# Kernel optimization log

Measured on AMD Instinct MI355X. Metric: run time of the kernel, lower is better.

## Reference

```python
import jax, jax.numpy as jnp
import numpy as np

N_NODES = 50000
N_EDGES = 600000
NUM_RELS = 5
IN_CH = 768
HID = 128
OUT_CH = 128
REL_DIM = 200


def _segment_softmax(scores, seg, n):
    # numerically stable softmax over variable-size segments (destination nodes)
    m = jax.ops.segment_max(scores, seg, num_segments=n)
    e = jnp.exp(scores - m[seg])
    s = jax.ops.segment_sum(e, seg, num_segments=n)
    return e / s[seg]


def _hgn_conv(x, edge_index, edge_type, W, Wr, a, Wres, rel_tab, final):
    # x: [N, h_in]; W: [h, h_in]; Wr: [h, rel_dim]; a: [3h]; rel_tab: [R, rel_dim]
    src = edge_index[0]
    dst = edge_index[1]
    n = x.shape[0]
    h = W.shape[0]
    Wx = x @ W.T                      # [N, h] (shared by x_i, x_j, messages)
    rel = rel_tab[edge_type] @ Wr.T   # [E, h]
    aA, aB, aC = a[:h], a[h:2 * h], a[2 * h:]
    # a([Wx_i | Wx_j | Wr rel]) decomposed to avoid materializing the concat
    score = Wx[dst] @ aA + Wx[src] @ aB + rel @ aC   # [E]
    alpha = jax.nn.leaky_relu(score, 0.2)
    alpha = _segment_softmax(alpha, dst, n)
    agg = jax.ops.segment_sum(Wx[src] * alpha[:, None], dst, num_segments=n)
    out = jax.nn.elu(agg + x @ Wres.T)
    if final:
        out = out / jnp.maximum(jnp.linalg.norm(out, axis=1, keepdims=True), 1e-12)
    return out, alpha


def setup_inputs() -> dict:
    key = jax.random.key(0)
    ks = jax.random.split(key, 20)
    s = 0.02
    return {
        "x": jax.random.normal(ks[0], (N_NODES, IN_CH), jnp.float32),
        "edge_index": jax.random.randint(ks[1], (2, N_EDGES), 0, N_NODES, jnp.int64 if jax.config.jax_enable_x64 else jnp.int32),
        "edge_type": jax.random.randint(ks[2], (N_EDGES,), 0, NUM_RELS, jnp.int64 if jax.config.jax_enable_x64 else jnp.int32),
        "l1_W": jax.random.normal(ks[3], (HID, IN_CH), jnp.float32) * s,
        "l1_b": jnp.zeros((HID,), jnp.float32),
        "l2_W": jax.random.normal(ks[4], (OUT_CH, HID), jnp.float32) * s,
        "l2_b": jnp.zeros((OUT_CH,), jnp.float32),
        "W1": jax.random.normal(ks[5], (HID, HID), jnp.float32) * s,
        "Wr1": jax.random.normal(ks[6], (HID, REL_DIM), jnp.float32) * s,
        "a1": jax.random.normal(ks[7], (3 * HID,), jnp.float32) * s,
        "Wres1": jax.random.normal(ks[8], (HID, HID), jnp.float32) * s,
        "rel1": jax.random.normal(ks[9], (NUM_RELS, REL_DIM), jnp.float32),
        "W2": jax.random.normal(ks[10], (HID, HID), jnp.float32) * s,
        "Wr2": jax.random.normal(ks[11], (HID, REL_DIM), jnp.float32) * s,
        "a2": jax.random.normal(ks[12], (3 * HID,), jnp.float32) * s,
        "Wres2": jax.random.normal(ks[13], (HID, HID), jnp.float32) * s,
        "rel2": jax.random.normal(ks[14], (NUM_RELS, REL_DIM), jnp.float32),
    }


def reference(x, edge_index, edge_type, l1_W, l1_b, l2_W, l2_b,
              W1, Wr1, a1, Wres1, rel1, W2, Wr2, a2, Wres2, rel2):
    out = jax.nn.leaky_relu(x @ l1_W.T + l1_b, 0.01)
    # layer 1 (dropout is identity in eval mode)
    out, alpha = _hgn_conv(out, edge_index, edge_type, W1, Wr1, a1, Wres1, rel1, final=False)
    # layer 2: original code blends alpha into self.alpha but weights messages
    # with its own (unblended) softmax alpha, so pre_alpha does not affect output
    out, _ = _hgn_conv(out, edge_index, edge_type, W2, Wr2, a2, Wres2, rel2, final=True)
    out = jax.nn.leaky_relu(out @ l2_W.T + l2_b, 0.01)
    return out
```

## Files before the change

### kernel.cpp

```cpp
#include <hip/hip_runtime.h>

namespace {

typedef unsigned short ushort_t;
typedef unsigned int uint_t;
typedef __attribute__((ext_vector_type(8))) short bf16x8;
typedef __attribute__((ext_vector_type(4))) float f32x4;

constexpr int N   = 50000;
constexpr int E   = 600000;
constexpr int NR  = 5;
constexpr int KIN = 768;
constexpr int H   = 128;
constexpr int RD  = 200;

__device__ inline ushort_t f2b(float f){
  uint_t u = __builtin_bit_cast(uint_t, f);
  uint_t r = (u + 0x7FFFu + ((u >> 16) & 1u)) >> 16;
  return (ushort_t)r;
}
__device__ inline float b2f_lo(uint_t u){ return __builtin_bit_cast(float, u << 16); }
__device__ inline float b2f_hi(uint_t u){ return __builtin_bit_cast(float, u & 0xFFFF0000u); }
__device__ inline float b2f_us(ushort_t h){ return __builtin_bit_cast(float, ((uint_t)h) << 16); }
__device__ inline uint_t cvtpk(float lo, float hi){
  uint_t r;
  asm("v_cvt_pk_bf16_f32 %0, %1, %2" : "=v"(r) : "v"(lo), "v"(hi));
  return r;
}

__global__ void prep_k(const float* __restrict__ l1W, const float* __restrict__ W1,
                       const float* __restrict__ R1, const float* __restrict__ W2,
                       const float* __restrict__ R2, const float* __restrict__ l2W,
                       ushort_t* __restrict__ wts, int* __restrict__ deg,
                       const int* __restrict__ edst,
                       const float* __restrict__ rel1, const float* __restrict__ Wr1,
                       const float* __restrict__ a1, float* __restrict__ sC1,
                       const float* __restrict__ rel2, const float* __restrict__ Wr2,
                       const float* __restrict__ a2, float* __restrict__ sC2){
  constexpr int S0 = H * KIN;
  constexpr int S1 = H * H;
  int b = blockIdx.x, tid = threadIdx.x;
  if (b < 704){
    int i = b * 256 + tid;
    float v;
    if (i < S0) v = l1W[i];
    else {
      int j = i - S0, seg = j >> 14, off = j & (S1 - 1);
      const float* srcs[5] = {W1, R1, W2, R2, l2W};
      v = srcs[seg][off];
    }
    wts[i] = f2b(v);
  } else if (b < 706){
    int L = b - 704;
    const float* rel = L ? rel2 : rel1;
    const float* Wr  = L ? Wr2  : Wr1;
    const float* a   = L ? a2   : a1;
    float*       sC  = L ? sC2  : sC1;
    __shared__ float red[256];
    int n = tid >> 1, half = tid & 1;
    float aC = a[256 + n];
    for (int r = 0; r < NR; ++r){
      float p = 0.f;
      for (int k = half * 100; k < half * 100 + 100; ++k)
        p += rel[r * RD + k] * Wr[n * RD + k];
      red[tid] = p * aC;
      __syncthreads();
      for (int s = 128; s > 0; s >>= 1){
        if (tid < s) red[tid] += red[tid + s];
        __syncthreads();
      }
      if (tid == 0) sC[r] = red[0];
      __syncthreads();
    }
  } else {
    int e = (b - 706) * 256 + tid;
    if (e < E) atomicAdd(&deg[edst[e]], 1);
  }
}

__global__ void scan1_k(const int* __restrict__ deg, int* __restrict__ chunk,
                        int* __restrict__ bsums, int n){
  __shared__ int s[256];
  int tid = threadIdx.x, i = blockIdx.x * 256 + tid;
  int v = (i < n) ? deg[i] : 0;
  s[tid] = v; __syncthreads();
  for (int off = 1; off < 256; off <<= 1){
    int t = (tid >= off) ? s[tid - off] : 0;
    __syncthreads();
    s[tid] += t;
    __syncthreads();
  }
  if (i < n) chunk[i] = s[tid] - v;
  if (tid == 255) bsums[blockIdx.x] = s[255];
}

__global__ void scan2_k(const int* __restrict__ bsums, int* __restrict__ boffs, int nb){
  __shared__ int s[256];
  int tid = threadIdx.x;
  int v = (tid < nb) ? bsums[tid] : 0;
  s[tid] = v; __syncthreads();
  for (int off = 1; off < 256; off <<= 1){
    int t = (tid >= off) ? s[tid - off] : 0;
    __syncthreads();
    s[tid] += t;
    __syncthreads();
  }
  if (tid < nb) boffs[tid] = s[tid] - v;
}

__global__ void scan3_k(int* __restrict__ rowptr, const int* __restrict__ boffs,
                        int* __restrict__ cursor, int n, int total){
  int i = blockIdx.x * 256 + threadIdx.x;
  if (i < n){
    int v = rowptr[i] + boffs[blockIdx.x];
    rowptr[i] = v; cursor[i] = v;
  }
  if (i == 0) rowptr[n] = total;
}

__global__ void fill_k(const int* __restrict__ src, const int* __restrict__ dst,
                       const int* __restrict__ et, int* __restrict__ cursor,
                       int* __restrict__ cpk){
  int e = blockIdx.x * 256 + threadIdx.x;
  if (e < E){
    int d = dst[e];
    int p = atomicAdd(&cursor[d], 1);
    cpk[p] = src[e] | (et[e] << 16);
  }
}

template<int K1, int M1, bool AFP32, bool NORM, bool STORE1, int M2>
__device__ __forceinline__ void gfused_impl(
    const void* __restrict__ Ap, const ushort_t* __restrict__ Wb1,
    const float* __restrict__ bias1,
    const ushort_t* __restrict__ WxG, const int* __restrict__ rowptr,
    const int* __restrict__ cpk, const float* __restrict__ sAi,
    const float* __restrict__ sBi, const float* __restrict__ sCi,
    ushort_t* __restrict__ out1,
    const ushort_t* __restrict__ Wb2, const float* __restrict__ vec2,
    void* __restrict__ out2, float* __restrict__ sAo, float* __restrict__ sBo, int M)
{
  constexpr int BK = 64;
  constexpr int NT = K1 / BK;
  constexpr int SP = 72;
  constexpr int CP = 136;
  __shared__ __align__(16) ushort_t U[128 * CP];
  __shared__ __align__(16) ushort_t Cs[64 * CP];
  ushort_t* const As  = U;
  ushort_t* const Bs  = U + 64 * SP;
  ushort_t* const B2s = U;
  const int tid  = threadIdx.x;
  const int wave = tid >> 6, lane = tid & 63;
  const int l15  = lane & 15, quad = lane >> 4;
  const int row0 = blockIdx.x * 64;

  if (M1 == 2){
    const int grp = tid >> 4;
    const int l   = tid & 15;
    const int gb  = tid & 48;
    #pragma unroll 1
    for (int nb = 0; nb < 4; ++nb){
      int lrow = nb * 16 + grp;
      int node = row0 + lrow;
      uint4 o = make_uint4(0, 0, 0, 0);
      if (node < M){
        int p0 = rowptr[node], p1 = rowptr[node + 1];
        int dg = p1 - p0;
        float sa = sAi[node];
        float m = -1e30f, ssum = 0.f;
        float a[8];
        #pragma unroll
        for (int j = 0; j < 8; ++j) a[j] = 0.f;
        for (int c0 = 0; c0 < dg; c0 += 16){
          int cnt = dg - c0; if (cnt > 16) cnt = 16;
          bool ok = l < cnt;
          int pk = cpk[p0 + c0 + (ok ? l : 0)];
          float s = sa + sBi[pk & 0xFFFF] + sCi[pk >> 16];
          s = s > 0.f ? s : 0.2f * s;
          float sv = ok ? s : -1e30f;
          #pragma unroll
          for (int off = 8; off > 0; off >>= 1) sv = fmaxf(sv, __shfl_xor(sv, off, 16));
          float mn = fmaxf(m, sv);
          float corr = __expf(m - mn);
          ssum *= corr;
          #pragma unroll
          for (int j = 0; j < 8; ++j) a[j] *= corr;
          float ev = ok ? __expf(s - mn) : 0.f;
          float es = ev;
          #pragma unroll
          for (int off = 8; off > 0; off >>= 1) es += __shfl_xor(es, off, 16);
          ssum += es;
          m = mn;
          int png = ok ? pk : 0;
          for (int e = 0; e < cnt; e += 4){
            int b0l = gb + e;
            int pe0 = __shfl(png, b0l,     64), pe1 = __shfl(png, b0l + 1, 64);
            int pe2 = __shfl(png, b0l + 2, 64), pe3 = __shfl(png, b0l + 3, 64);
            float e0 = __shfl(ev, b0l,     64), e1 = __shfl(ev, b0l + 1, 64);
            float e2 = __shfl(ev, b0l + 2, 64), e3 = __shfl(ev, b0l + 3, 64);
            uint4 u0 = *reinterpret_cast<const uint4*>(WxG + (size_t)(pe0 & 0xFFFF) * 128 + l * 8);
            uint4 u1 = *reinterpret_cast<const uint4*>(WxG + (size_t)(pe1 & 0xFFFF) * 128 + l * 8);
            uint4 u2 = *reinterpret_cast<const uint4*>(WxG + (size_t)(pe2 & 0xFFFF) * 128 + l * 8);
            uint4 u3 = *reinterpret_cast<const uint4*>(WxG + (size_t)(pe3 & 0xFFFF) * 128 + l * 8);
            a[0] += e0 * b2f_lo(u0.x); a[1] += e0 * b2f_hi(u0.x);
            a[2] += e0 * b2f_lo(u0.y); a[3] += e0 * b2f_hi(u0.y);
            a[4] += e0 * b2f_lo(u0.z); a[5] += e0 * b2f_hi(u0.z);
            a[6] += e0 * b2f_lo(u0.w); a[7] += e0 * b2f_hi(u0.w);
            a[0] += e1 * b2f_lo(u1.x); a[1] += e1 * b2f_hi(u1.x);
            a[2] += e1 * b2f_lo(u1.y); a[3] += e1 * b2f_hi(u1.y);
            a[4] += e1 * b2f_lo(u1.z); a[5] += e1 * b2f_hi(u1.z);
            a[6] += e1 * b2f_lo(u1.w); a[7] += e1 * b2f_hi(u1.w);
            a[0] += e2 * b2f_lo(u2.x); a[1] += e2 * b2f_hi(u2.x);
            a[2] += e2 * b2f_lo(u2.y); a[3] += e2 * b2f_hi(u2.y);
            a[4] += e2 * b2f_lo(u2.z); a[5] += e2 * b2f_hi(u2.z);
            a[6] += e2 * b2f_lo(u2.w); a[7] += e2 * b2f_hi(u2.w);
            a[0] += e3 * b2f_lo(u3.x); a[1] += e3 * b2f_hi(u3.x);
            a[2] += e3 * b2f_lo(u3.y); a[3] += e3 * b2f_hi(u3.y);
            a[4] += e3 * b2f_lo(u3.z); a[5] += e3 * b2f_hi(u3.z);
            a[6] += e3 * b2f_lo(u3.w); a[7] += e3 * b2f_hi(u3.w);
          }
        }
        float inv = (dg > 0) ? 1.f / ssum : 0.f;
        o.x = cvtpk(a[0] * inv, a[1] * inv);
        o.y = cvtpk(a[2] * inv, a[3] * inv);
        o.z = cvtpk(a[4] * inv, a[5] * inv);
        o.w = cvtpk(a[6] * inv, a[7] * inv);
      }
      *reinterpret_cast<uint4*>(&Cs[lrow * CP + l * 8]) = o;
    }
  }

  f32x4 acc[8];
  #pragma unroll
  for (int t = 0; t < 8; ++t) acc[t] = (f32x4){0.f, 0.f, 0.f, 0.f};

  const int ar = tid >> 2, aq = tid & 3;
  const int agrow = row0 + ar;
  const bool aok = agrow < M;
  const int awoff = ar * SP + aq * 16;
  const int bn = tid >> 1, bs = (tid & 1) * 32;
  const ushort_t* bsrc = Wb1 + (size_t)bn * K1 + bs;

  float4 pf0, pf1, pf2, pf3;
  uint4  pu0, pu1;
  uint4  pb0, pb1, pb2, pb3;
  pf0 = pf1 = pf2 = pf3 = make_float4(0.f, 0.f, 0.f, 0.f);
  pu0 = pu1 = make_uint4(0, 0, 0, 0);

#define ISSUE_A(kk) do{ if (aok){                                               \
    if constexpr (AFP32){                                                       \
      const float* ap_ = (const float*)Ap + (size_t)agrow * K1 + (kk) + aq * 16; \
      pf0 = *reinterpret_cast<const float4*>(ap_);                              \
      pf1 = *reinterpret_cast<const float4*>(ap_ + 4);                          \
      pf2 = *reinterpret_cast<const float4*>(ap_ + 8);                          \
      pf3 = *reinterpret_cast<const float4*>(ap_ + 12);                         \
    } else {                                                                    \
      const ushort_t* apb_ = (const ushort_t*)Ap + (size_t)agrow * K1 + (kk) + aq * 16; \
      pu0 = *reinterpret_cast<const uint4*>(apb_);                              \
      pu1 = *reinterpret_cast<const uint4*>(apb_ + 8);                          \
    } } }while(0)

#define ISSUE_B(kk) do{                                                         \
    pb0 = *reinterpret_cast<const uint4*>(bsrc + (kk));                         \
    pb1 = *reinterpret_cast<const uint4*>(bsrc + (kk) + 8);                     \
    pb2 = *reinterpret_cast<const uint4*>(bsrc + (kk) + 16);                    \
    pb3 = *reinterpret_cast<const uint4*>(bsrc + (kk) + 24);                    \
  }while(0)

#define WRITE_AB() do{                                                          \
    uint4 av0_, av1_;                                                           \
    if constexpr (AFP32){                                                       \
      av0_.x = cvtpk(pf0.x, pf0.y); av0_.y = cvtpk(pf0.z, pf0.w);               \
      av0_.z = cvtpk(pf1.x, pf1.y); av0_.w = cvtpk(pf1.z, pf1.w);               \
      av1_.x = cvtpk(pf2.x, pf2.y); av1_.y = cvtpk(pf2.z, pf2.w);               \
      av1_.z = cvtpk(pf3.x, pf3.y); av1_.w = cvtpk(pf3.z, pf3.w);               \
    } else { av0_ = pu0; av1_ = pu1; }                                          \
    *reinterpret_cast<uint4*>(&As[awoff])     = av0_;                           \
    *reinterpret_cast<uint4*>(&As[awoff + 8]) = av1_;                           \
    *reinterpret_cast<uint4*>(&Bs[bn * SP + bs])      = pb0;                    \
    *reinterpret_cast<uint4*>(&Bs[bn * SP + bs + 8])  = pb1;                    \
    *reinterpret_cast<uint4*>(&Bs[bn * SP + bs + 16]) = pb2;                    \
    *reinterpret_cast<uint4*>(&Bs[bn * SP + bs + 24]) = pb3;                    \
  }while(0)

  ISSUE_A(0); ISSUE_B(0);
  for (int t = 0; t < NT; ++t){
    WRITE_AB();
    __syncthreads();
    if (t + 1 < NT){ ISSUE_A((t + 1) * BK); ISSUE_B((t + 1) * BK); }
    bf16x8 af0 = *reinterpret_cast<const bf16x8*>(&As[(wave * 16 + l15) * SP + quad * 8]);
    bf16x8 af1 = *reinterpret_cast<const bf16x8*>(&As[(wave * 16 + l15) * SP + 32 + quad * 8]);
    #pragma unroll
    for (int tt = 0; tt < 8; ++tt){
      bf16x8 b0 = *reinterpret_cast<const bf16x8*>(&Bs[(tt * 16 + l15) * SP + quad * 8]);
      acc[tt] = __builtin_amdgcn_mfma_f32_16x16x32_bf16(af0, b0, acc[tt], 0, 0, 0);
      bf16x8 b1 = *reinterpret_cast<const bf16x8*>(&Bs[(tt * 16 + l15) * SP + 32 + quad * 8]);
      acc[tt] = __builtin_amdgcn_mfma_f32_16x16x32_bf16(af1, b1, acc[tt], 0, 0, 0);
    }
    __syncthreads();
  }
#undef ISSUE_A
#undef ISSUE_B
#undef WRITE_AB

  uint4 wreg[8];
  #pragma unroll
  for (int i = 0; i < 8; ++i){
    int idx = tid + 256 * i;
    int rr = idx >> 4, c8 = idx & 15;
    wreg[i] = *reinterpret_cast<const uint4*>(Wb2 + (size_t)rr * 128 + c8 * 8);
  }

  float vv[8][4];
  #pragma unroll
  for (int t = 0; t < 8; ++t){
    #pragma unroll
    for (int r = 0; r < 4; ++r){
      int lr  = wave * 16 + quad * 4 + r;
      int col = t * 16 + l15;
      float v = acc[t][r];
      if (M1 == 1){
        v += bias1[col];
        v = v > 0.f ? v : 0.01f * v;
      } else {
        v += b2f_us(Cs[lr * CP + col]);
        v = v > 0.f ? v : __expf(v) - 1.f;
      }
      vv[t][r] = v;
    }
  }
  #pragma unroll
  for (int i = 0; i < 8; ++i){
    int idx = tid + 256 * i;
    int rr = idx >> 4, c8 = idx & 15;
    *reinterpret_cast<uint4*>(&B2s[rr * CP + c8 * 8]) = wreg[i];
  }
  if (NORM){
    #pragma unroll
    for (int r = 0; r < 4; ++r){
      float ss = 0.f;
      #pragma unroll
      for (int t = 0; t < 8; ++t) ss += vv[t][r] * vv[t][r];
      #pragma unroll
      for (int off = 1; off < 16; off <<= 1) ss += __shfl_xor(ss, off, 64);
      float sc = 1.f / fmaxf(sqrtf(ss), 1e-12f);
      #pragma unroll
      for (int t = 0; t < 8; ++t) vv[t][r] *= sc;
    }
  }
  #pragma unroll
  for (int t = 0; t < 8; t += 2){
    #pragma unroll
    for (int r = 0; r < 4; ++r){
      int lr  = wave * 16 + quad * 4 + r;
      int c0  = t * 16 + l15, c1 = c0 + 16;
      uint_t pr = cvtpk(vv[t][r], vv[t + 1][r]);
      Cs[lr * CP + c0] = (ushort_t)pr;
      Cs[lr * CP + c1] = (ushort_t)(pr >> 16);
      if (STORE1){
        int grow = row0 + lr;
        if (grow < M){
          out1[(size_t)grow * 128 + c0] = (ushort_t)pr;
          out1[(size_t)grow * 128 + c1] = (ushort_t)(pr >> 16);
        }
      }
    }
  }
  __syncthreads();

  #pragma unroll
  for (int t = 0; t < 8; ++t) acc[t] = (f32x4){0.f, 0.f, 0.f, 0.f};
  #pragma unroll
  for (int kk = 0; kk < 4; ++kk){
    bf16x8 af2 = *reinterpret_cast<const bf16x8*>(&Cs[(wave * 16 + l15) * CP + kk * 32 + quad * 8]);
    #pragma unroll
    for (int t = 0; t < 8; ++t){
      bf16x8 bfr = *reinterpret_cast<const bf16x8*>(&B2s[(t * 16 + l15) * CP + kk * 32 + quad * 8]);
      acc[t] = __builtin_amdgcn_mfma_f32_16x16x32_bf16(af2, bfr, acc[t], 0, 0, 0);
    }
  }

  if (M2 == 1){
    #pragma unroll
    for (int t = 0; t < 8; ++t){
      #pragma unroll
      for (int r = 0; r < 4; ++r){
        int grow = row0 + wave * 16 + quad * 4 + r;
        if (grow >= M) continue;
        int col = t * 16 + l15;
        float v = acc[t][r] + vec2[col];
        v = v > 0.f ? v : 0.01f * v;
        ((float*)out2)[(size_t)grow * 128 + col] = v;
      }
    }
  } else {
    #pragma unroll
    for (int t = 0; t < 8; t += 2){
      #pragma unroll
      for (int r = 0; r < 4; ++r){
        int grow = row0 + wave * 16 + quad * 4 + r;
        if (grow >= M) continue;
        int c0 = t * 16 + l15;
        uint_t pr = cvtpk(acc[t][r], acc[t + 1][r]);
        ((ushort_t*)out2)[(size_t)grow * 128 + c0]      = (ushort_t)pr;
        ((ushort_t*)out2)[(size_t)grow * 128 + c0 + 16] = (ushort_t)(pr >> 16);
      }
    }
    #pragma unroll
    for (int r = 0; r < 4; ++r){
      float pa = 0.f, pb = 0.f;
      #pragma unroll
      for (int t = 0; t < 8; ++t){
        int col = t * 16 + l15;
        pa += acc[t][r] * vec2[col];
        pb += acc[t][r] * vec2[128 + col];
      }
      #pragma unroll
      for (int off = 1; off < 16; off <<= 1){
        pa += __shfl_xor(pa, off, 64);
        pb += __shfl_xor(pb, off, 64);
      }
      int grow = row0 + wave * 16 + quad * 4 + r;
      if (l15 == r && grow < M){ sAo[grow] = pa; sBo[grow] = pb; }
    }
  }
}

__global__ __launch_bounds__(256) void g1_k(
    const void* Ap, const ushort_t* Wb1, const float* bias1,
    ushort_t* out1, const ushort_t* Wb2, const float* vec2,
    void* out2, float* sAo, float* sBo, int M){
  gfused_impl<KIN, 1, true, false, true, 3>(Ap, Wb1, bias1, nullptr, nullptr,
      nullptr, nullptr, nullptr, nullptr, out1, Wb2, vec2, out2, sAo, sBo, M);
}
__global__ __launch_bounds__(256) void g2_k(
    const void* Ap, const ushort_t* Wb1,
    const ushort_t* WxG, const int* rowptr, const int* cpk,
    const float* sAi, const float* sBi, const float* sCi,
    ushort_t* out1, const ushort_t* Wb2, const float* vec2,
    void* out2, float* sAo, float* sBo, int M){
  gfused_impl<H, 2, false, false, true, 3>(Ap, Wb1, nullptr, WxG, rowptr, cpk,
      sAi, sBi, sCi, out1, Wb2, vec2, out2, sAo, sBo, M);
}
__global__ __launch_bounds__(256) void g3_k(
    const void* Ap, const ushort_t* Wb1,
    const ushort_t* WxG, const int* rowptr, const int* cpk,
    const float* sAi, const float* sBi, const float* sCi,
    const ushort_t* Wb2, const float* vec2, void* out2, int M){
  gfused_impl<H, 2, false, true, false, 1>(Ap, Wb1, nullptr, WxG, rowptr, cpk,
      sAi, sBi, sCi, nullptr, Wb2, vec2, out2, nullptr, nullptr, M);
}

}

extern "C" void kernel_launch(void* const* d_in, const int* in_sizes, int n_in,
                              void* d_out, int out_size, void* d_ws, size_t ws_size,
                              hipStream_t stream)
{
  const float* x     = (const float*)d_in[0];
  const int*   eidx  = (const int*)d_in[1];
  const int*   et    = (const int*)d_in[2];
  const float* l1W   = (const float*)d_in[3];
  const float* l1b   = (const float*)d_in[4];
  const float* l2W   = (const float*)d_in[5];
  const float* l2b   = (const float*)d_in[6];
  const float* W1    = (const float*)d_in[7];
  const float* Wr1   = (const float*)d_in[8];
  const float* a1    = (const float*)d_in[9];
  const float* Wres1 = (const float*)d_in[10];
  const float* rel1  = (const float*)d_in[11];
  const float* W2    = (const float*)d_in[12];
  const float* Wr2   = (const float*)d_in[13];
  const float* a2    = (const float*)d_in[14];
  const float* Wres2 = (const float*)d_in[15];
  const float* rel2  = (const float*)d_in[16];
  float* outp = (float*)d_out;

  const int* esrc = eidx;
  const int* edst = eidx + E;

  float* f = (float*)d_ws;
  size_t o = 0;
  float* sA1  = f + o; o += N;
  float* sB1  = f + o; o += N;
  float* sA2  = f + o; o += N;
  float* sB2  = f + o; o += N;
  float* sC1  = f + o; o += 8;
  float* sC2  = f + o; o += 8;
  ushort_t* us = (ushort_t*)(f + o);
  size_t ou = 0;
  ushort_t* b0   = us + ou; ou += (size_t)N * H;
  ushort_t* b1   = us + ou; ou += (size_t)N * H;
  ushort_t* WxA  = us + ou; ou += (size_t)N * H;
  ushort_t* WxB  = us + ou; ou += (size_t)N * H;
  ushort_t* wtsb = us + ou; ou += (size_t)H * KIN + 5 * H * H;
  ushort_t* l1Wb = wtsb;
  ushort_t* W1b  = wtsb + H * KIN;
  ushort_t* R1b  = W1b + H * H;
  ushort_t* W2b  = R1b + H * H;
  ushort_t* R2b  = W2b + H * H;
  ushort_t* l2Wb = R2b + H * H;
  if (ou & 1) ou += 1;
  int* wi = (int*)(us + ou);
  size_t oi = 0;
  int* deg    = wi + oi; oi += N;
  int* rowptr = wi + oi; oi += N + 1;
  int* cursor = wi + oi; oi += N;
  int* bsums  = wi + oi; oi += 256;
  int* boffs  = wi + oi; oi += 256;
  int* cpk    = wi + oi; oi += E;

  const int EB    = (E + 255) / 256;
  const int NB256 = (N + 255) / 256;
  const int GB    = (N + 63) / 64;

  hipMemsetAsync(deg, 0, (size_t)N * sizeof(int), stream);
  prep_k<<<706 + EB, 256, 0, stream>>>(l1W, W1, Wres1, W2, Wres2, l2W, wtsb, deg,
                                       edst, rel1, Wr1, a1, sC1, rel2, Wr2, a2, sC2);
  scan1_k<<<NB256, 256, 0, stream>>>(deg, rowptr, bsums, N);
  scan2_k<<<1, 256, 0, stream>>>(bsums, boffs, NB256);
  scan3_k<<<NB256, 256, 0, stream>>>(rowptr, boffs, cursor, N, E);
  fill_k<<<EB, 256, 0, stream>>>(esrc, edst, et, cursor, cpk);

  g1_k<<<GB, 256, 0, stream>>>(x, l1Wb, l1b, b0, W1b, a1, WxA, sA1, sB1, N);

  g2_k<<<GB, 256, 0, stream>>>(b0, R1b, WxA, rowptr, cpk, sA1, sB1, sC1,
                               b1, W2b, a2, WxB, sA2, sB2, N);

  g3_k<<<GB, 256, 0, stream>>>(b1, R2b, WxB, rowptr, cpk, sA2, sB2, sC2,
                               l2Wb, l2b, outp, N);
}
```

Measured before the change: 481.7 us.

## Specialize GEMM kernels, merge scan stages, and restructure residual GEMM ordering

Merges scan2 and scan3 so every block redundantly scans the block sums, removing one kernel launch. Splits the templated fused GEMM into a dedicated layer-1 kernel with a K tile of 128 and wider prefetch, and a layer-2/3 kernel. The layer-2/3 kernel loads the A fragments directly from global memory into registers and runs the residual GEMM before the edge aggregation, so the tiled K loop and its staging go away. Output stores are coalesced through shared memory as 16-byte vectors. In exchange it uses more registers and LDS, and every scan block repeats the same small scan.

```diff
diff --git a/kernel.cpp b/kernel.cpp
--- a/kernel.cpp
+++ b/kernel.cpp
@@ -94,7 +94,8 @@
   if (tid == 255) bsums[blockIdx.x] = s[255];
 }
 
-__global__ void scan2_k(const int* __restrict__ bsums, int* __restrict__ boffs, int nb){
+__global__ void scan3_k(int* __restrict__ rowptr, const int* __restrict__ bsums,
+                        int* __restrict__ cursor, int n, int total, int nb){
   __shared__ int s[256];
   int tid = threadIdx.x;
   int v = (tid < nb) ? bsums[tid] : 0;
@@ -105,15 +106,12 @@
     s[tid] += t;
     __syncthreads();
   }
-  if (tid < nb) boffs[tid] = s[tid] - v;
-}
-
-__global__ void scan3_k(int* __restrict__ rowptr, const int* __restrict__ boffs,
-                        int* __restrict__ cursor, int n, int total){
-  int i = blockIdx.x * 256 + threadIdx.x;
+  int bown = (blockIdx.x < nb) ? bsums[blockIdx.x] : 0;
+  int add  = s[blockIdx.x] - bown;
+  int i = blockIdx.x * 256 + tid;
   if (i < n){
-    int v = rowptr[i] + boffs[blockIdx.x];
-    rowptr[i] = v; cursor[i] = v;
+    int val = rowptr[i] + add;
+    rowptr[i] = val; cursor[i] = val;
   }
   if (i == 0) rowptr[n] = total;
 }
@@ -129,10 +127,167 @@
   }
 }
 
-template<int K1, int M1, bool AFP32, bool NORM, bool STORE1, int M2>
-__device__ __forceinline__ void gfused_impl(
-    const void* __restrict__ Ap, const ushort_t* __restrict__ Wb1,
-    const float* __restrict__ bias1,
+__global__ __launch_bounds__(256) void g1_k(
+    const float* __restrict__ Ap, const ushort_t* __restrict__ Wb1,
+    const float* __restrict__ bias1, ushort_t* __restrict__ out1,
+    const ushort_t* __restrict__ Wb2, const float* __restrict__ vec2,
+    ushort_t* __restrict__ out2, float* __restrict__ sAo, float* __restrict__ sBo, int M)
+{
+  constexpr int K1 = KIN;
+  constexpr int BK = 128;
+  constexpr int NT = K1 / BK;
+  constexpr int SP = 136;
+  __shared__ __align__(16) ushort_t U[192 * SP];
+  __shared__ __align__(16) ushort_t Cs[64 * SP];
+  ushort_t* const As  = U;
+  ushort_t* const Bs  = U + 64 * SP;
+  ushort_t* const B2s = U;
+  const int tid  = threadIdx.x;
+  const int wave = tid >> 6, lane = tid & 63;
+  const int l15  = lane & 15, quad = lane >> 4;
+  const int row0 = blockIdx.x * 64;
+
+  f32x4 acc[8];
+  #pragma unroll
+  for (int t = 0; t < 8; ++t) acc[t] = (f32x4){0.f, 0.f, 0.f, 0.f};
+
+  const int ar = tid >> 2, aseg = (tid & 3) * 32;
+  int agrow = row0 + ar; if (agrow >= M) agrow = M - 1;
+  const float* asrc = Ap + (size_t)agrow * K1 + aseg;
+  const int bn = tid >> 1, bh = (tid & 1) * 64;
+  const ushort_t* bsrc = Wb1 + (size_t)bn * K1 + bh;
+
+  float4 pa[8]; uint4 pb[8];
+#define ISSUE(kk) do{                                                           \
+    _Pragma("unroll") for (int j_ = 0; j_ < 8; ++j_)                            \
+      pa[j_] = *reinterpret_cast<const float4*>(asrc + (kk) + j_ * 4);          \
+    _Pragma("unroll") for (int j_ = 0; j_ < 8; ++j_)                            \
+      pb[j_] = *reinterpret_cast<const uint4*>(bsrc + (kk) + j_ * 8);           \
+  }while(0)
+#define WRITE_AB() do{                                                          \
+    _Pragma("unroll") for (int j_ = 0; j_ < 4; ++j_){                           \
+      uint4 av_;                                                                \
+      av_.x = cvtpk(pa[2*j_].x, pa[2*j_].y);  av_.y = cvtpk(pa[2*j_].z, pa[2*j_].w); \
+      av_.z = cvtpk(pa[2*j_+1].x, pa[2*j_+1].y); av_.w = cvtpk(pa[2*j_+1].z, pa[2*j_+1].w); \
+      *reinterpret_cast<uint4*>(&As[ar * SP + aseg + j_ * 8]) = av_;            \
+    }                                                                           \
+    _Pragma("unroll") for (int j_ = 0; j_ < 8; ++j_)                            \
+      *reinterpret_cast<uint4*>(&Bs[bn * SP + bh + j_ * 8]) = pb[j_];           \
+  }while(0)
+
+  ISSUE(0);
+  for (int t = 0; t < NT; ++t){
+    WRITE_AB();
+    __syncthreads();
+    if (t + 1 < NT) ISSUE((t + 1) * BK);
+    #pragma unroll
+    for (int kk = 0; kk < 4; ++kk){
+      bf16x8 af = *reinterpret_cast<const bf16x8*>(&As[(wave * 16 + l15) * SP + kk * 32 + quad * 8]);
+      #pragma unroll
+      for (int tt = 0; tt < 8; ++tt){
+        bf16x8 bfr = *reinterpret_cast<const bf16x8*>(&Bs[(tt * 16 + l15) * SP + kk * 32 + quad * 8]);
+        acc[tt] = __builtin_amdgcn_mfma_f32_16x16x32_bf16(af, bfr, acc[tt], 0, 0, 0);
+      }
+    }
+    __syncthreads();
+  }
+#undef ISSUE
+#undef WRITE_AB
+
+  uint4 wreg[8];
+  #pragma unroll
+  for (int i = 0; i < 8; ++i){
+    int idx = tid + 256 * i;
+    int rr = idx >> 4, c8 = idx & 15;
+    wreg[i] = *reinterpret_cast<const uint4*>(Wb2 + (size_t)rr * 128 + c8 * 8);
+  }
+
+  const int lr0 = wave * 16 + quad * 4;
+  float vv[8][4];
+  #pragma unroll
+  for (int t = 0; t < 8; ++t){
+    #pragma unroll
+    for (int r = 0; r < 4; ++r){
+      int col = t * 16 + l15;
+      float v = acc[t][r] + bias1[col];
+      vv[t][r] = v > 0.f ? v : 0.01f * v;
+    }
+  }
+  #pragma unroll
+  for (int i = 0; i < 8; ++i){
+    int idx = tid + 256 * i;
+    int rr = idx >> 4, c8 = idx & 15;
+    *reinterpret_cast<uint4*>(&B2s[rr * SP + c8 * 8]) = wreg[i];
+  }
+  #pragma unroll
+  for (int t = 0; t < 8; t += 2){
+    #pragma unroll
+    for (int r = 0; r < 4; ++r){
+      int row = lr0 + r;
+      int c0 = t * 16 + l15, c1 = c0 + 16;
+      uint_t pr = cvtpk(vv[t][r], vv[t + 1][r]);
+      Cs[row * SP + c0] = (ushort_t)pr;
+      Cs[row * SP + c1] = (ushort_t)(pr >> 16);
+    }
+  }
+  __syncthreads();
+
+  #pragma unroll
+  for (int i = 0; i < 4; ++i){
+    int idx = tid + 256 * i;
+    int row = idx >> 4, c8 = idx & 15;
+    int g = row0 + row;
+    if (g < M)
+      *reinterpret_cast<uint4*>(out1 + (size_t)g * 128 + c8 * 8) =
+          *reinterpret_cast<const uint4*>(&Cs[row * SP + c8 * 8]);
+  }
+
+  #pragma unroll
+  for (int t = 0; t < 8; ++t) acc[t] = (f32x4){0.f, 0.f, 0.f, 0.f};
+  #pragma unroll
+  for (int kk = 0; kk < 4; ++kk){
+    bf16x8 af2 = *reinterpret_cast<const bf16x8*>(&Cs[(wave * 16 + l15) * SP + kk * 32 + quad * 8]);
+    #pragma unroll
+    for (int t = 0; t < 8; ++t){
+      bf16x8 bfr = *reinterpret_cast<const bf16x8*>(&B2s[(t * 16 + l15) * SP + kk * 32 + quad * 8]);
+      acc[t] = __builtin_amdgcn_mfma_f32_16x16x32_bf16(af2, bfr, acc[t], 0, 0, 0);
+    }
+  }
+
+  #pragma unroll
+  for (int t = 0; t < 8; t += 2){
+    #pragma unroll
+    for (int r = 0; r < 4; ++r){
+      int grow = row0 + lr0 + r;
+      if (grow >= M) continue;
+      int c0 = t * 16 + l15;
+      uint_t pr = cvtpk(acc[t][r], acc[t + 1][r]);
+      out2[(size_t)grow * 128 + c0]      = (ushort_t)pr;
+      out2[(size_t)grow * 128 + c0 + 16] = (ushort_t)(pr >> 16);
+    }
+  }
+  #pragma unroll
+  for (int r = 0; r < 4; ++r){
+    float pa2 = 0.f, pb2 = 0.f;
+    #pragma unroll
+    for (int t = 0; t < 8; ++t){
+      int col = t * 16 + l15;
+      pa2 += acc[t][r] * vec2[col];
+      pb2 += acc[t][r] * vec2[128 + col];
+    }
+    #pragma unroll
+    for (int off = 1; off < 16; off <<= 1){
+      pa2 += __shfl_xor(pa2, off, 64);
+      pb2 += __shfl_xor(pb2, off, 64);
+    }
+    int grow = row0 + lr0 + r;
+    if (l15 == r && grow < M){ sAo[grow] = pa2; sBo[grow] = pb2; }
+  }
+}
+
+template<bool NORM, bool STORE1, int M2>
+__device__ __forceinline__ void g23_impl(
+    const ushort_t* __restrict__ Ap, const ushort_t* __restrict__ Wb1,
     const ushort_t* __restrict__ WxG, const int* __restrict__ rowptr,
     const int* __restrict__ cpk, const float* __restrict__ sAi,
     const float* __restrict__ sBi, const float* __restrict__ sCi,
@@ -140,24 +295,45 @@
     const ushort_t* __restrict__ Wb2, const float* __restrict__ vec2,
     void* __restrict__ out2, float* __restrict__ sAo, float* __restrict__ sBo, int M)
 {
-  constexpr int BK = 64;
-  constexpr int NT = K1 / BK;
-  constexpr int SP = 72;
-  constexpr int CP = 136;
-  __shared__ __align__(16) ushort_t U[128 * CP];
-  __shared__ __align__(16) ushort_t Cs[64 * CP];
-  ushort_t* const As  = U;
-  ushort_t* const Bs  = U + 64 * SP;
-  ushort_t* const B2s = U;
+  constexpr int SP = 136;
+  __shared__ __align__(16) ushort_t U[128 * SP];
+  __shared__ __align__(16) ushort_t Cs[64 * SP];
   const int tid  = threadIdx.x;
   const int wave = tid >> 6, lane = tid & 63;
   const int l15  = lane & 15, quad = lane >> 4;
   const int row0 = blockIdx.x * 64;
 
-  if (M1 == 2){
-    const int grp = tid >> 4;
-    const int l   = tid & 15;
-    const int gb  = tid & 48;
+  int arl = row0 + wave * 16 + l15; if (arl >= M) arl = M - 1;
+  const ushort_t* arow = Ap + (size_t)arl * 128 + quad * 8;
+  bf16x8 af0 = *reinterpret_cast<const bf16x8*>(arow);
+  bf16x8 af1 = *reinterpret_cast<const bf16x8*>(arow + 32);
+  bf16x8 af2 = *reinterpret_cast<const bf16x8*>(arow + 64);
+  bf16x8 af3 = *reinterpret_cast<const bf16x8*>(arow + 96);
+
+  {
+    const int bn = tid >> 1, bh = (tid & 1) * 64;
+    const ushort_t* bsrc = Wb1 + (size_t)bn * 128 + bh;
+    #pragma unroll
+    for (int j = 0; j < 8; ++j)
+      *reinterpret_cast<uint4*>(&U[bn * SP + bh + j * 8]) =
+          *reinterpret_cast<const uint4*>(bsrc + j * 8);
+  }
+  __syncthreads();
+
+  f32x4 acc[8];
+  #pragma unroll
+  for (int t = 0; t < 8; ++t) acc[t] = (f32x4){0.f, 0.f, 0.f, 0.f};
+  #pragma unroll
+  for (int t = 0; t < 8; ++t){
+    const ushort_t* bp = &U[(t * 16 + l15) * SP + quad * 8];
+    acc[t] = __builtin_amdgcn_mfma_f32_16x16x32_bf16(af0, *reinterpret_cast<const bf16x8*>(bp),      acc[t], 0, 0, 0);
+    acc[t] = __builtin_amdgcn_mfma_f32_16x16x32_bf16(af1, *reinterpret_cast<const bf16x8*>(bp + 32), acc[t], 0, 0, 0);
+    acc[t] = __builtin_amdgcn_mfma_f32_16x16x32_bf16(af2, *reinterpret_cast<const bf16x8*>(bp + 64), acc[t], 0, 0, 0);
+    acc[t] = __builtin_amdgcn_mfma_f32_16x16x32_bf16(af3, *reinterpret_cast<const bf16x8*>(bp + 96), acc[t], 0, 0, 0);
+  }
+
+  {
+    const int grp = tid >> 4, l = tid & 15, gb = tid & 48;
     #pragma unroll 1
     for (int nb = 0; nb < 4; ++nb){
       int lrow = nb * 16 + grp;
@@ -226,82 +402,9 @@
         o.z = cvtpk(a[4] * inv, a[5] * inv);
         o.w = cvtpk(a[6] * inv, a[7] * inv);
       }
-      *reinterpret_cast<uint4*>(&Cs[lrow * CP + l * 8]) = o;
-    }
-  }
-
-  f32x4 acc[8];
-  #pragma unroll
-  for (int t = 0; t < 8; ++t) acc[t] = (f32x4){0.f, 0.f, 0.f, 0.f};
-
-  const int ar = tid >> 2, aq = tid & 3;
-  const int agrow = row0 + ar;
-  const bool aok = agrow < M;
-  const int awoff = ar * SP + aq * 16;
-  const int bn = tid >> 1, bs = (tid & 1) * 32;
-  const ushort_t* bsrc = Wb1 + (size_t)bn * K1 + bs;
-
-  float4 pf0, pf1, pf2, pf3;
-  uint4  pu0, pu1;
-  uint4  pb0, pb1, pb2, pb3;
-  pf0 = pf1 = pf2 = pf3 = make_float4(0.f, 0.f, 0.f, 0.f);
-  pu0 = pu1 = make_uint4(0, 0, 0, 0);
-
-#define ISSUE_A(kk) do{ if (aok){                                               \
-    if constexpr (AFP32){                                                       \
-      const float* ap_ = (const float*)Ap + (size_t)agrow * K1 + (kk) + aq * 16; \
-      pf0 = *reinterpret_cast<const float4*>(ap_);                              \
-      pf1 = *reinterpret_cast<const float4*>(ap_ + 4);                          \
-      pf2 = *reinterpret_cast<const float4*>(ap_ + 8);                          \
-      pf3 = *reinterpret_cast<const float4*>(ap_ + 12);                         \
-    } else {                                                                    \
-      const ushort_t* apb_ = (const ushort_t*)Ap + (size_t)agrow * K1 + (kk) + aq * 16; \
-      pu0 = *reinterpret_cast<const uint4*>(apb_);                              \
-      pu1 = *reinterpret_cast<const uint4*>(apb_ + 8);                          \
-    } } }while(0)
-
-#define ISSUE_B(kk) do{                                                         \
-    pb0 = *reinterpret_cast<const uint4*>(bsrc + (kk));                         \
-    pb1 = *reinterpret_cast<const uint4*>(bsrc + (kk) + 8);                     \
-    pb2 = *reinterpret_cast<const uint4*>(bsrc + (kk) + 16);                    \
-    pb3 = *reinterpret_cast<const uint4*>(bsrc + (kk) + 24);                    \
-  }while(0)
-
-#define WRITE_AB() do{                                                          \
-    uint4 av0_, av1_;                                                           \
-    if constexpr (AFP32){                                                       \
-      av0_.x = cvtpk(pf0.x, pf0.y); av0_.y = cvtpk(pf0.z, pf0.w);               \
-      av0_.z = cvtpk(pf1.x, pf1.y); av0_.w = cvtpk(pf1.z, pf1.w);               \
-      av1_.x = cvtpk(pf2.x, pf2.y); av1_.y = cvtpk(pf2.z, pf2.w);               \
-      av1_.z = cvtpk(pf3.x, pf3.y); av1_.w = cvtpk(pf3.z, pf3.w);               \
-    } else { av0_ = pu0; av1_ = pu1; }                                          \
-    *reinterpret_cast<uint4*>(&As[awoff])     = av0_;                           \
-    *reinterpret_cast<uint4*>(&As[awoff + 8]) = av1_;                           \
-    *reinterpret_cast<uint4*>(&Bs[bn * SP + bs])      = pb0;                    \
-    *reinterpret_cast<uint4*>(&Bs[bn * SP + bs + 8])  = pb1;                    \
-    *reinterpret_cast<uint4*>(&Bs[bn * SP + bs + 16]) = pb2;                    \
-    *reinterpret_cast<uint4*>(&Bs[bn * SP + bs + 24]) = pb3;                    \
-  }while(0)
-
-  ISSUE_A(0); ISSUE_B(0);
-  for (int t = 0; t < NT; ++t){
-    WRITE_AB();
-    __syncthreads();
-    if (t + 1 < NT){ ISSUE_A((t + 1) * BK); ISSUE_B((t + 1) * BK); }
-    bf16x8 af0 = *reinterpret_cast<const bf16x8*>(&As[(wave * 16 + l15) * SP + quad * 8]);
-    bf16x8 af1 = *reinterpret_cast<const bf16x8*>(&As[(wave * 16 + l15) * SP + 32 + quad * 8]);
-    #pragma unroll
-    for (int tt = 0; tt < 8; ++tt){
-      bf16x8 b0 = *reinterpret_cast<const bf16x8*>(&Bs[(tt * 16 + l15) * SP + quad * 8]);
-      acc[tt] = __builtin_amdgcn_mfma_f32_16x16x32_bf16(af0, b0, acc[tt], 0, 0, 0);
-      bf16x8 b1 = *reinterpret_cast<const bf16x8*>(&Bs[(tt * 16 + l15) * SP + 32 + quad * 8]);
-      acc[tt] = __builtin_amdgcn_mfma_f32_16x16x32_bf16(af1, b1, acc[tt], 0, 0, 0);
-    }
-    __syncthreads();
-  }
-#undef ISSUE_A
-#undef ISSUE_B
-#undef WRITE_AB
+      *reinterpret_cast<uint4*>(&Cs[lrow * SP + l * 8]) = o;
+    }
+  }
 
   uint4 wreg[8];
   #pragma unroll
@@ -310,30 +413,25 @@
     int rr = idx >> 4, c8 = idx & 15;
     wreg[i] = *reinterpret_cast<const uint4*>(Wb2 + (size_t)rr * 128 + c8 * 8);
   }
-
-  float vv[8][4];
-  #pragma unroll
-  for (int t = 0; t < 8; ++t){
-    #pragma unroll
-    for (int r = 0; r < 4; ++r){
-      int lr  = wave * 16 + quad * 4 + r;
-      int col = t * 16 + l15;
-      float v = acc[t][r];
-      if (M1 == 1){
-        v += bias1[col];
-        v = v > 0.f ? v : 0.01f * v;
-      } else {
-        v += b2f_us(Cs[lr * CP + col]);
-        v = v > 0.f ? v : __expf(v) - 1.f;
-      }
-      vv[t][r] = v;
-    }
-  }
+  __syncthreads();
+
   #pragma unroll
   for (int i = 0; i < 8; ++i){
     int idx = tid + 256 * i;
     int rr = idx >> 4, c8 = idx & 15;
-    *reinterpret_cast<uint4*>(&B2s[rr * CP + c8 * 8]) = wreg[i];
+    *reinterpret_cast<uint4*>(&U[rr * SP + c8 * 8]) = wreg[i];
+  }
+
+  const int lr0 = wave * 16 + quad * 4;
+  float vv[8][4];
+  #pragma unroll
+  for (int t = 0; t < 8; ++t){
+    #pragma unroll
+    for (int r = 0; r < 4; ++r){
+      int col = t * 16 + l15;
+      float v = acc[t][r] + b2f_us(Cs[(lr0 + r) * SP + col]);
+      vv[t][r] = v > 0.f ? v : __expf(v) - 1.f;
+    }
   }
   if (NORM){
     #pragma unroll
@@ -352,31 +450,36 @@
   for (int t = 0; t < 8; t += 2){
     #pragma unroll
     for (int r = 0; r < 4; ++r){
-      int lr  = wave * 16 + quad * 4 + r;
-      int c0  = t * 16 + l15, c1 = c0 + 16;
+      int row = lr0 + r;
+      int c0 = t * 16 + l15, c1 = c0 + 16;
       uint_t pr = cvtpk(vv[t][r], vv[t + 1][r]);
-      Cs[lr * CP + c0] = (ushort_t)pr;
-      Cs[lr * CP + c1] = (ushort_t)(pr >> 16);
-      if (STORE1){
-        int grow = row0 + lr;
-        if (grow < M){
-          out1[(size_t)grow * 128 + c0] = (ushort_t)pr;
-          out1[(size_t)grow * 128 + c1] = (ushort_t)(pr >> 16);
-        }
-      }
+      Cs[row * SP + c0] = (ushort_t)pr;
+      Cs[row * SP + c1] = (ushort_t)(pr >> 16);
     }
   }
   __syncthreads();
 
+  if (STORE1){
+    #pragma unroll
+    for (int i = 0; i < 4; ++i){
+      int idx = tid + 256 * i;
+      int row = idx >> 4, c8 = idx & 15;
+      int g = row0 + row;
+      if (g < M)
+        *reinterpret_cast<uint4*>(out1 + (size_t)g * 128 + c8 * 8) =
+            *reinterpret_cast<const uint4*>(&Cs[row * SP + c8 * 8]);
+    }
+  }
+
   #pragma unroll
   for (int t = 0; t < 8; ++t) acc[t] = (f32x4){0.f, 0.f, 0.f, 0.f};
   #pragma unroll
   for (int kk = 0; kk < 4; ++kk){
-    bf16x8 af2 = *reinterpret_cast<const bf16x8*>(&Cs[(wave * 16 + l15) * CP + kk * 32 + quad * 8]);
+    bf16x8 a2f = *reinterpret_cast<const bf16x8*>(&Cs[(wave * 16 + l15) * SP + kk * 32 + quad * 8]);
     #pragma unroll
     for (int t = 0; t < 8; ++t){
-      bf16x8 bfr = *reinterpret_cast<const bf16x8*>(&B2s[(t * 16 + l15) * CP + kk * 32 + quad * 8]);
-      acc[t] = __builtin_amdgcn_mfma_f32_16x16x32_bf16(af2, bfr, acc[t], 0, 0, 0);
+      bf16x8 bfr = *reinterpret_cast<const bf16x8*>(&U[(t * 16 + l15) * SP + kk * 32 + quad * 8]);
+      acc[t] = __builtin_amdgcn_mfma_f32_16x16x32_bf16(a2f, bfr, acc[t], 0, 0, 0);
     }
   }
 
@@ -385,7 +488,7 @@
     for (int t = 0; t < 8; ++t){
       #pragma unroll
       for (int r = 0; r < 4; ++r){
-        int grow = row0 + wave * 16 + quad * 4 + r;
+        int grow = row0 + lr0 + r;
         if (grow >= M) continue;
         int col = t * 16 + l15;
         float v = acc[t][r] + vec2[col];
@@ -398,7 +501,7 @@
     for (int t = 0; t < 8; t += 2){
       #pragma unroll
       for (int r = 0; r < 4; ++r){
-        int grow = row0 + wave * 16 + quad * 4 + r;
+        int grow = row0 + lr0 + r;
         if (grow >= M) continue;
         int c0 = t * 16 + l15;
         uint_t pr = cvtpk(acc[t][r], acc[t + 1][r]);
@@ -408,47 +511,40 @@
     }
     #pragma unroll
     for (int r = 0; r < 4; ++r){
-      float pa = 0.f, pb = 0.f;
+      float pa2 = 0.f, pb2 = 0.f;
       #pragma unroll
       for (int t = 0; t < 8; ++t){
         int col = t * 16 + l15;
-        pa += acc[t][r] * vec2[col];
-        pb += acc[t][r] * vec2[128 + col];
+        pa2 += acc[t][r] * vec2[col];
+        pb2 += acc[t][r] * vec2[128 + col];
       }
       #pragma unroll
       for (int off = 1; off < 16; off <<= 1){
-        pa += __shfl_xor(pa, off, 64);
-        pb += __shfl_xor(pb, off, 64);
+        pa2 += __shfl_xor(pa2, off, 64);
+        pb2 += __shfl_xor(pb2, off, 64);
       }
-      int grow = row0 + wave * 16 + quad * 4 + r;
-      if (l15 == r && grow < M){ sAo[grow] = pa; sBo[grow] = pb; }
-    }
-  }
-}
-
-__global__ __launch_bounds__(256) void g1_k(
-    const void* Ap, const ushort_t* Wb1, const float* bias1,
-    ushort_t* out1, const ushort_t* Wb2, const float* vec2,
-    void* out2, float* sAo, float* sBo, int M){
-  gfused_impl<KIN, 1, true, false, true, 3>(Ap, Wb1, bias1, nullptr, nullptr,
-      nullptr, nullptr, nullptr, nullptr, out1, Wb2, vec2, out2, sAo, sBo, M);
-}
+      int grow = row0 + lr0 + r;
+      if (l15 == r && grow < M){ sAo[grow] = pa2; sBo[grow] = pb2; }
+    }
+  }
+}
+
 __global__ __launch_bounds__(256) void g2_k(
-    const void* Ap, const ushort_t* Wb1,
+    const ushort_t* Ap, const ushort_t* Wb1,
     const ushort_t* WxG, const int* rowptr, const int* cpk,
     const float* sAi, const float* sBi, const float* sCi,
     ushort_t* out1, const ushort_t* Wb2, const float* vec2,
     void* out2, float* sAo, float* sBo, int M){
-  gfused_impl<H, 2, false, false, true, 3>(Ap, Wb1, nullptr, WxG, rowptr, cpk,
-      sAi, sBi, sCi, out1, Wb2, vec2, out2, sAo, sBo, M);
+  g23_impl<false, true, 3>(Ap, Wb1, WxG, rowptr, cpk, sAi, sBi, sCi,
+                           out1, Wb2, vec2, out2, sAo, sBo, M);
 }
 __global__ __launch_bounds__(256) void g3_k(
-    const void* Ap, const ushort_t* Wb1,
+    const ushort_t* Ap, const ushort_t* Wb1,
     const ushort_t* WxG, const int* rowptr, const int* cpk,
     const float* sAi, const float* sBi, const float* sCi,
     const ushort_t* Wb2, const float* vec2, void* out2, int M){
-  gfused_impl<H, 2, false, true, false, 1>(Ap, Wb1, nullptr, WxG, rowptr, cpk,
-      sAi, sBi, sCi, nullptr, Wb2, vec2, out2, nullptr, nullptr, M);
+  g23_impl<true, false, 1>(Ap, Wb1, WxG, rowptr, cpk, sAi, sBi, sCi,
+                           nullptr, Wb2, vec2, out2, nullptr, nullptr, M);
 }
 
 }
@@ -518,8 +614,7 @@
   prep_k<<<706 + EB, 256, 0, stream>>>(l1W, W1, Wres1, W2, Wres2, l2W, wtsb, deg,
                                        edst, rel1, Wr1, a1, sC1, rel2, Wr2, a2, sC2);
   scan1_k<<<NB256, 256, 0, stream>>>(deg, rowptr, bsums, N);
-  scan2_k<<<1, 256, 0, stream>>>(bsums, boffs, NB256);
-  scan3_k<<<NB256, 256, 0, stream>>>(rowptr, boffs, cursor, N, E);
+  scan3_k<<<NB256, 256, 0, stream>>>(rowptr, bsums, cursor, N, E, NB256);
   fill_k<<<EB, 256, 0, stream>>>(esrc, edst, et, cursor, cpk);
 
   g1_k<<<GB, 256, 0, stream>>>(x, l1Wb, l1b, b0, W1b, a1, WxA, sA1, sB1, N);
```

Result: slower. 590.3 us (+22.5%).
